# Kernel tuning notes

Measured on AMD Instinct MI355X. Metric: run time of the kernel, lower is better.

The kernel has to match this reference:

```python
import jax, jax.numpy as jnp
import numpy as np

TOP_K = 2

def setup_inputs() -> dict:
    key = jax.random.key(0)
    ks = jax.random.split(key, 5)
    B, S, H, F, E = 2, 1024, 2048, 4096, 8
    scale_h = 1.0 / np.sqrt(H)
    scale_f = 1.0 / np.sqrt(F)
    return {
        "hidden_states": jax.random.normal(ks[0], (B, S, H), dtype=jnp.float32),
        # nn.Linear weight layout is [out, in]
        "gate_w": jax.random.normal(ks[1], (E, H), dtype=jnp.float32) * scale_h,
        "w_gate": jax.random.normal(ks[2], (E, F, H), dtype=jnp.float32) * scale_h,
        "w_up": jax.random.normal(ks[3], (E, F, H), dtype=jnp.float32) * scale_h,
        "w_down": jax.random.normal(ks[4], (E, H, F), dtype=jnp.float32) * scale_f,
    }

def reference(hidden_states, gate_w, w_gate, w_up, w_down):
    B, S, H = hidden_states.shape
    E = gate_w.shape[0]
    x = hidden_states.reshape(-1, H)                     # [T, H]
    T = x.shape[0]
    # Router: softmax -> top-k -> renormalize
    router_logits = x @ gate_w.T                         # [T, E]
    routing_weights = jax.nn.softmax(router_logits, axis=-1)
    topk_w, topk_i = jax.lax.top_k(routing_weights, TOP_K)  # [T, k]
    topk_w = topk_w / jnp.sum(topk_w, axis=-1, keepdims=True)
    # Dense [T, E] combine weights (zero for non-selected experts);
    # equivalent math to the per-expert gather/scatter loop.
    dense_w = jnp.zeros((T, E), dtype=x.dtype).at[
        jnp.arange(T)[:, None], topk_i].set(topk_w)
    # SwiGLU experts, batched over E (grouped GEMM expressed densely)
    g = jnp.einsum('th,efh->tef', x, w_gate)             # [T, E, F]
    u = jnp.einsum('th,efh->tef', x, w_up)               # [T, E, F]
    h = jax.nn.silu(g) * u                               # [T, E, F]
    y = jnp.einsum('tef,ehf->teh', h, w_down)            # [T, E, H]
    out = jnp.einsum('te,teh->th', dense_w, y)           # [T, H]
    return out.reshape(B, S, H)
```

## Files before the change

kernel.cpp:

```cpp
#include <hip/hip_runtime.h>
#include <hip/hip_bf16.h>


#define T_TOK 2048
#define H_DIM 2048
#define F_DIM 4096
#define E_NUM 8
#define NPAIR (T_TOK * 2)

typedef __attribute__((ext_vector_type(8))) short short8;
typedef __attribute__((ext_vector_type(4))) float f32x4;

__device__ __forceinline__ unsigned short f2bf(float f) {
    unsigned u = __builtin_bit_cast(unsigned, f);
    u = (u + 0x7FFFu + ((u >> 16) & 1u)) >> 16;
    return (unsigned short)u;
}

__device__ __forceinline__ uint4 pack8(float4 a, float4 b) {
    uint4 o;
    o.x = f2bf(a.x) | ((unsigned)f2bf(a.y) << 16);
    o.y = f2bf(a.z) | ((unsigned)f2bf(a.w) << 16);
    o.z = f2bf(b.x) | ((unsigned)f2bf(b.y) << 16);
    o.w = f2bf(b.z) | ((unsigned)f2bf(b.w) << 16);
    return o;
}

__device__ __forceinline__ uint2 pack4(float4 a) {
    uint2 o;
    o.x = f2bf(a.x) | ((unsigned)f2bf(a.y) << 16);
    o.y = f2bf(a.z) | ((unsigned)f2bf(a.w) << 16);
    return o;
}

__device__ __forceinline__ void gload16(const void* g, void* s) {
    __builtin_amdgcn_global_load_lds(
        (const __attribute__((address_space(1))) unsigned int*)g,
        (__attribute__((address_space(3))) unsigned int*)s, 16, 0, 0);
}

__global__ void k_router(const float* __restrict__ x, const float* __restrict__ gw,
                         ushort* __restrict__ xb,
                         int2* __restrict__ eidx, float2* __restrict__ ew,
                         int* __restrict__ cnt) {
    int t = blockIdx.x * 4 + (threadIdx.x >> 6);
    int lane = threadIdx.x & 63;
    const float* xr = x + (size_t)t * H_DIM;
    ushort* xbr = xb + (size_t)t * H_DIM;

    #pragma unroll
    for (int j = 0; j < 4; j++) {
        int idx = (j * 64 + lane) * 8;
        const float4* p = (const float4*)(xr + idx);
        uint2 lo = pack4(p[0]), hi = pack4(p[1]);
        *(uint4*)(xbr + idx) = make_uint4(lo.x, lo.y, hi.x, hi.y);
    }

    float l[E_NUM];
    #pragma unroll
    for (int e = 0; e < E_NUM; e++) {
        const float* wr = gw + (size_t)e * H_DIM;
        float acc = 0.f;
        for (int i = lane; i < H_DIM; i += 64) acc += xr[i] * wr[i];
        #pragma unroll
        for (int o = 32; o; o >>= 1) acc += __shfl_xor(acc, o);
        l[e] = acc;
    }
    if (lane == 0) {
        int e0 = 0;
        #pragma unroll
        for (int e = 1; e < E_NUM; e++) if (l[e] > l[e0]) e0 = e;
        int e1 = -1;
        #pragma unroll
        for (int e = 0; e < E_NUM; e++) {
            if (e == e0) continue;
            if (e1 < 0 || l[e] > l[e1]) e1 = e;
        }
        float s1 = expf(l[e1] - l[e0]);
        float w0 = 1.f / (1.f + s1);
        float w1 = s1 * w0;
        eidx[t] = make_int2(e0, e1);
        ew[t]   = make_float2(w0, w1);
        atomicAdd(&cnt[e0], 1);
        atomicAdd(&cnt[e1], 1);
    }
}

__global__ void k_offfill(const int* __restrict__ cnt, int* __restrict__ off,
                          const int2* __restrict__ eidx,
                          int* __restrict__ ptok, int2* __restrict__ inv) {
    __shared__ int soff[E_NUM];
    __shared__ int scnt[E_NUM];
    if (threadIdx.x == 0) {
        int s = 0;
        for (int e = 0; e < E_NUM; e++) { soff[e] = s; off[e] = s; s += cnt[e]; scnt[e] = 0; }
        off[E_NUM] = s;
    }
    __syncthreads();
    for (int t = threadIdx.x; t < T_TOK; t += blockDim.x) {
        int2 e = eidx[t];
        int p0 = soff[e.x] + atomicAdd(&scnt[e.x], 1);
        ptok[p0] = t;
        int p1 = soff[e.y] + atomicAdd(&scnt[e.y], 1);
        ptok[p1] = t;
        inv[t] = make_int2(p0, p1);
    }
}

__global__ __launch_bounds__(512, 4) void k_gemm1(
        const ushort* __restrict__ xb, const float* __restrict__ wg,
        const float* __restrict__ wu, const int* __restrict__ ptok,
        const int* __restrict__ off, ushort* __restrict__ hbuf) {
    __shared__ __align__(16) ushort As[256 * 64];
    __shared__ __align__(16) ushort Bg[64 * 64];
    __shared__ __align__(16) ushort Bu[64 * 64];

    int e = blockIdx.y >> 3, mt = blockIdx.y & 7;
    int base = off[e], ne = off[e + 1] - base;
    int row0 = mt * 256;
    if (row0 >= ne) return;
    int nb = blockIdx.x * 64;

    int tid = threadIdx.x;
    int wv = tid >> 6, l = tid & 63;
    int lr = l & 15, lk = l >> 4;
    int wm = wv >> 1, wn = wv & 1;

    int wvu = __builtin_amdgcn_readfirstlane(wv);
    const ushort* srcA[4];
    int sslot = 8 * ((l & 7) ^ ((l >> 3) & 7));
    #pragma unroll
    for (int c = 0; c < 4; c++) {
        int r = (wvu * 4 + c) * 8 + (l >> 3);
        int pp = base + min(row0 + r, ne - 1);
        srcA[c] = xb + (size_t)ptok[pp] * H_DIM + sslot;
    }

    int brow = tid >> 3, bs = tid & 7;
    const float* wgrow = wg + ((size_t)e * F_DIM + nb + brow) * H_DIM + bs * 8;
    const float* wurow = wu + ((size_t)e * F_DIM + nb + brow) * H_DIM + bs * 8;
    int bo = brow * 64 + (((bs * 16) ^ ((brow & 7) << 4)) >> 1);

    int rsw = (lr & 7) << 4;

    f32x4 accg[4][2] = {}; f32x4 accu[4][2] = {};

    for (int kb = 0; kb < H_DIM; kb += 64) {
        __syncthreads();
        #pragma unroll
        for (int c = 0; c < 4; c++)
            gload16(srcA[c] + kb, (ushort*)As + (wvu * 4 + c) * 512);
        float4 g0 = *(const float4*)(wgrow + kb);
        float4 g1 = *(const float4*)(wgrow + kb + 4);
        *(uint4*)(&Bg[bo]) = pack8(g0, g1);
        float4 u0 = *(const float4*)(wurow + kb);
        float4 u1 = *(const float4*)(wurow + kb + 4);
        *(uint4*)(&Bu[bo]) = pack8(u0, u1);
        __syncthreads();

        #pragma unroll
        for (int kk = 0; kk < 2; kk++) {
            int kby = kk * 64 + lk * 16;
            short8 a[4];
            #pragma unroll
            for (int m = 0; m < 4; m++) {
                int row = wm * 64 + m * 16 + lr;
                a[m] = *(const short8*)(&As[(row * 128 + (kby ^ rsw)) >> 1]);
            }
            #pragma unroll
            for (int n = 0; n < 2; n++) {
                int rowb = wn * 32 + n * 16 + lr;
                int boff = (rowb * 128 + (kby ^ rsw)) >> 1;
                short8 bg8 = *(const short8*)(&Bg[boff]);
                short8 bu8 = *(const short8*)(&Bu[boff]);
                #pragma unroll
                for (int m = 0; m < 4; m++) {
                    accg[m][n] = __builtin_amdgcn_mfma_f32_16x16x32_bf16(a[m], bg8, accg[m][n], 0, 0, 0);
                    accu[m][n] = __builtin_amdgcn_mfma_f32_16x16x32_bf16(a[m], bu8, accu[m][n], 0, 0, 0);
                }
            }
        }
    }

    #pragma unroll
    for (int m = 0; m < 4; m++) {
        #pragma unroll
        for (int r = 0; r < 4; r++) {
            int lrow = wm * 64 + m * 16 + lk * 4 + r;
            if (row0 + lrow < ne) {
                size_t rb = (size_t)(base + row0 + lrow) * F_DIM + nb;
                #pragma unroll
                for (int n = 0; n < 2; n++) {
                    float g = accg[m][n][r], u = accu[m][n][r];
                    float hv = g / (1.f + __expf(-g)) * u;
                    hbuf[rb + wn * 32 + n * 16 + lr] = f2bf(hv);
                }
            }
        }
    }
}

__global__ __launch_bounds__(512, 2) void k_gemm2(
        const ushort* __restrict__ hbuf, const float* __restrict__ wd,
        const int* __restrict__ off, float* __restrict__ ybuf) {
    __shared__ __align__(16) ushort As[256 * 64];
    __shared__ __align__(16) ushort Bs[128 * 64];

    int e = blockIdx.y >> 3, mt = blockIdx.y & 7;
    int base = off[e], ne = off[e + 1] - base;
    int row0 = mt * 256;
    if (row0 >= ne) return;
    int nb = blockIdx.x * 128;

    int tid = threadIdx.x;
    int wv = tid >> 6, l = tid & 63;
    int lr = l & 15, lk = l >> 4;
    int wm = wv >> 1, wn = wv & 1;

    int wvu = __builtin_amdgcn_readfirstlane(wv);
    const ushort* srcA[4];
    int sslot = 8 * ((l & 7) ^ ((l >> 3) & 7));
    #pragma unroll
    for (int c = 0; c < 4; c++) {
        int r = (wvu * 4 + c) * 8 + (l >> 3);
        int pp = base + min(row0 + r, ne - 1);
        srcA[c] = hbuf + (size_t)pp * F_DIM + sslot;
    }

    int brow = tid >> 2, bs = tid & 3;
    const float* wdrow = wd + ((size_t)e * H_DIM + nb + brow) * F_DIM + bs * 16;
    int bsw = (brow & 7) << 4;
    int bo0 = brow * 64 + (((bs * 32) ^ bsw) >> 1);
    int bo1 = brow * 64 + (((bs * 32 + 16) ^ bsw) >> 1);

    int rsw = (lr & 7) << 4;

    f32x4 acc[4][4] = {};

    for (int kb = 0; kb < F_DIM; kb += 64) {
        __syncthreads();
        #pragma unroll
        for (int c = 0; c < 4; c++)
            gload16(srcA[c] + kb, (ushort*)As + (wvu * 4 + c) * 512);
        float4 b0 = *(const float4*)(wdrow + kb);
        float4 b1 = *(const float4*)(wdrow + kb + 4);
        float4 b2 = *(const float4*)(wdrow + kb + 8);
        float4 b3 = *(const float4*)(wdrow + kb + 12);
        *(uint4*)(&Bs[bo0]) = pack8(b0, b1);
        *(uint4*)(&Bs[bo1]) = pack8(b2, b3);
        __syncthreads();

        #pragma unroll
        for (int kk = 0; kk < 2; kk++) {
            int kby = kk * 64 + lk * 16;
            short8 a[4];
            #pragma unroll
            for (int m = 0; m < 4; m++) {
                int row = wm * 64 + m * 16 + lr;
                a[m] = *(const short8*)(&As[(row * 128 + (kby ^ rsw)) >> 1]);
            }
            #pragma unroll
            for (int n = 0; n < 4; n++) {
                int rowb = wn * 64 + n * 16 + lr;
                short8 b8 = *(const short8*)(&Bs[(rowb * 128 + (kby ^ rsw)) >> 1]);
                #pragma unroll
                for (int m = 0; m < 4; m++)
                    acc[m][n] = __builtin_amdgcn_mfma_f32_16x16x32_bf16(a[m], b8, acc[m][n], 0, 0, 0);
            }
        }
    }

    #pragma unroll
    for (int m = 0; m < 4; m++) {
        #pragma unroll
        for (int r = 0; r < 4; r++) {
            int lrow = wm * 64 + m * 16 + lk * 4 + r;
            if (row0 + lrow < ne) {
                float* yrow = ybuf + (size_t)(base + row0 + lrow) * H_DIM + nb;
                #pragma unroll
                for (int n = 0; n < 4; n++)
                    yrow[wn * 64 + n * 16 + lr] = acc[m][n][r];
            }
        }
    }
}

__global__ void k_combine(const float* __restrict__ ybuf,
                          const float2* __restrict__ ew,
                          const int2* __restrict__ inv,
                          float* __restrict__ out) {
    int t = blockIdx.x;
    float2 w = ew[t];
    int2 pp = inv[t];
    const float4* y0 = (const float4*)(ybuf + (size_t)pp.x * H_DIM);
    const float4* y1 = (const float4*)(ybuf + (size_t)pp.y * H_DIM);
    float4* o = (float4*)(out + (size_t)t * H_DIM);
    for (int j = threadIdx.x; j < H_DIM / 4; j += blockDim.x) {
        float4 a = y0[j], b = y1[j];
        float4 r;
        r.x = w.x * a.x + w.y * b.x;
        r.y = w.x * a.y + w.y * b.y;
        r.z = w.x * a.z + w.y * b.z;
        r.w = w.x * a.w + w.y * b.w;
        o[j] = r;
    }
}

extern "C" void kernel_launch(void* const* d_in, const int* in_sizes, int n_in,
                              void* d_out, int out_size, void* d_ws, size_t ws_size,
                              hipStream_t stream) {
    const float* x  = (const float*)d_in[0];
    const float* gw = (const float*)d_in[1];
    const float* wg = (const float*)d_in[2];
    const float* wu = (const float*)d_in[3];
    const float* wd = (const float*)d_in[4];
    float* out = (float*)d_out;

    char* ws = (char*)d_ws;
    size_t o = 0;
    ushort* xb   = (ushort*)(ws + o); o += (size_t)T_TOK * H_DIM * 2;
    ushort* hbuf = (ushort*)(ws + o); o += (size_t)NPAIR * F_DIM * 2;
    float*  ybuf = (float*) (ws + o); o += (size_t)NPAIR * H_DIM * 4;
    int*    ptok = (int*)   (ws + o); o += NPAIR * 4;
    int2*   eidx = (int2*)  (ws + o); o += T_TOK * 8;
    float2* ew   = (float2*)(ws + o); o += T_TOK * 8;
    int2*   inv  = (int2*)  (ws + o); o += T_TOK * 8;
    int*    cnt  = (int*)   (ws + o); o += 256;
    int*    off  = (int*)   (ws + o); o += 256;

    hipMemsetAsync(cnt, 0, 256, stream);

    k_router <<<T_TOK / 4, 256, 0, stream>>>(x, gw, xb, eidx, ew, cnt);
    k_offfill<<<1, 256, 0, stream>>>(cnt, off, eidx, ptok, inv);

    dim3 g1(F_DIM / 64, E_NUM * 8);
    k_gemm1<<<g1, 512, 0, stream>>>(xb, wg, wu, ptok, off, hbuf);
    dim3 g2(H_DIM / 128, E_NUM * 8);
    k_gemm2<<<g2, 512, 0, stream>>>(hbuf, wd, off, ybuf);
    k_combine<<<T_TOK, 256, 0, stream>>>(ybuf, ew, inv, out);
}
```

Before: 555.9 us.

## Split gate/up GEMM into two sequential phases with wider N tile

The fused gate/up GEMM is split into two sequential passes inside each block, each computing a 128-wide N tile with one B buffer. The gate result is stored as bf16 to hbuf and read back during the up pass to apply SiLU and multiply. Each A tile is reused across twice as many columns per pass, and accumulator register pressure stays about the same. The cost is that the gathered A rows are loaded twice (once per phase) and there is an extra global round-trip through hbuf. The gate value is also rounded to bf16 before SiLU.

```diff
diff --git a/kernel.cpp b/kernel.cpp
--- a/kernel.cpp
+++ b/kernel.cpp
@@ -15,6 +15,11 @@
     unsigned u = __builtin_bit_cast(unsigned, f);
     u = (u + 0x7FFFu + ((u >> 16) & 1u)) >> 16;
     return (unsigned short)u;
+}
+
+__device__ __forceinline__ float bf2f(unsigned short us) {
+    unsigned u = ((unsigned)us) << 16;
+    return __builtin_bit_cast(float, u);
 }
 
 __device__ __forceinline__ uint4 pack8(float4 a, float4 b) {
@@ -112,14 +117,13 @@
         const float* __restrict__ wu, const int* __restrict__ ptok,
         const int* __restrict__ off, ushort* __restrict__ hbuf) {
     __shared__ __align__(16) ushort As[256 * 64];
-    __shared__ __align__(16) ushort Bg[64 * 64];
-    __shared__ __align__(16) ushort Bu[64 * 64];
+    __shared__ __align__(16) ushort Bs[128 * 64];
 
     int e = blockIdx.y >> 3, mt = blockIdx.y & 7;
     int base = off[e], ne = off[e + 1] - base;
     int row0 = mt * 256;
     if (row0 >= ne) return;
-    int nb = blockIdx.x * 64;
+    int nb = blockIdx.x * 128;
 
     int tid = threadIdx.x;
     int wv = tid >> 6, l = tid & 63;
@@ -136,64 +140,70 @@
         srcA[c] = xb + (size_t)ptok[pp] * H_DIM + sslot;
     }
 
-    int brow = tid >> 3, bs = tid & 7;
-    const float* wgrow = wg + ((size_t)e * F_DIM + nb + brow) * H_DIM + bs * 8;
-    const float* wurow = wu + ((size_t)e * F_DIM + nb + brow) * H_DIM + bs * 8;
-    int bo = brow * 64 + (((bs * 16) ^ ((brow & 7) << 4)) >> 1);
+    int brow = tid >> 2, bs = tid & 3;
+    size_t woff = ((size_t)e * F_DIM + nb + brow) * H_DIM + bs * 16;
+    int bsw = (brow & 7) << 4;
+    int bo0 = brow * 64 + (((bs * 32) ^ bsw) >> 1);
+    int bo1 = brow * 64 + (((bs * 32 + 16) ^ bsw) >> 1);
 
     int rsw = (lr & 7) << 4;
 
-    f32x4 accg[4][2] = {}; f32x4 accu[4][2] = {};
-
-    for (int kb = 0; kb < H_DIM; kb += 64) {
-        __syncthreads();
-        #pragma unroll
-        for (int c = 0; c < 4; c++)
-            gload16(srcA[c] + kb, (ushort*)As + (wvu * 4 + c) * 512);
-        float4 g0 = *(const float4*)(wgrow + kb);
-        float4 g1 = *(const float4*)(wgrow + kb + 4);
-        *(uint4*)(&Bg[bo]) = pack8(g0, g1);
-        float4 u0 = *(const float4*)(wurow + kb);
-        float4 u1 = *(const float4*)(wurow + kb + 4);
-        *(uint4*)(&Bu[bo]) = pack8(u0, u1);
-        __syncthreads();
-
-        #pragma unroll
-        for (int kk = 0; kk < 2; kk++) {
-            int kby = kk * 64 + lk * 16;
-            short8 a[4];
-            #pragma unroll
-            for (int m = 0; m < 4; m++) {
-                int row = wm * 64 + m * 16 + lr;
-                a[m] = *(const short8*)(&As[(row * 128 + (kby ^ rsw)) >> 1]);
-            }
-            #pragma unroll
-            for (int n = 0; n < 2; n++) {
-                int rowb = wn * 32 + n * 16 + lr;
-                int boff = (rowb * 128 + (kby ^ rsw)) >> 1;
-                short8 bg8 = *(const short8*)(&Bg[boff]);
-                short8 bu8 = *(const short8*)(&Bu[boff]);
+    #pragma unroll 1
+    for (int ph = 0; ph < 2; ph++) {
+        const float* wrow = (ph ? wu : wg) + woff;
+        f32x4 acc[4][4] = {};
+
+        for (int kb = 0; kb < H_DIM; kb += 64) {
+            __syncthreads();
+            #pragma unroll
+            for (int c = 0; c < 4; c++)
+                gload16(srcA[c] + kb, (ushort*)As + (wvu * 4 + c) * 512);
+            float4 b0 = *(const float4*)(wrow + kb);
+            float4 b1 = *(const float4*)(wrow + kb + 4);
+            float4 b2 = *(const float4*)(wrow + kb + 8);
+            float4 b3 = *(const float4*)(wrow + kb + 12);
+            *(uint4*)(&Bs[bo0]) = pack8(b0, b1);
+            *(uint4*)(&Bs[bo1]) = pack8(b2, b3);
+            __syncthreads();
+
+            #pragma unroll
+            for (int kk = 0; kk < 2; kk++) {
+                int kby = kk * 64 + lk * 16;
+                short8 a[4];
                 #pragma unroll
                 for (int m = 0; m < 4; m++) {
-                    accg[m][n] = __builtin_amdgcn_mfma_f32_16x16x32_bf16(a[m], bg8, accg[m][n], 0, 0, 0);
-                    accu[m][n] = __builtin_amdgcn_mfma_f32_16x16x32_bf16(a[m], bu8, accu[m][n], 0, 0, 0);
+                    int row = wm * 64 + m * 16 + lr;
+                    a[m] = *(const short8*)(&As[(row * 128 + (kby ^ rsw)) >> 1]);
                 }
-            }
-        }
-    }
-
-    #pragma unroll
-    for (int m = 0; m < 4; m++) {
-        #pragma unroll
-        for (int r = 0; r < 4; r++) {
-            int lrow = wm * 64 + m * 16 + lk * 4 + r;
-            if (row0 + lrow < ne) {
-                size_t rb = (size_t)(base + row0 + lrow) * F_DIM + nb;
                 #pragma unroll
-                for (int n = 0; n < 2; n++) {
-                    float g = accg[m][n][r], u = accu[m][n][r];
-                    float hv = g / (1.f + __expf(-g)) * u;
-                    hbuf[rb + wn * 32 + n * 16 + lr] = f2bf(hv);
+                for (int n = 0; n < 4; n++) {
+                    int rowb = wn * 64 + n * 16 + lr;
+                    short8 b8 = *(const short8*)(&Bs[(rowb * 128 + (kby ^ rsw)) >> 1]);
+                    #pragma unroll
+                    for (int m = 0; m < 4; m++)
+                        acc[m][n] = __builtin_amdgcn_mfma_f32_16x16x32_bf16(a[m], b8, acc[m][n], 0, 0, 0);
+                }
+            }
+        }
+
+        #pragma unroll
+        for (int m = 0; m < 4; m++) {
+            #pragma unroll
+            for (int r = 0; r < 4; r++) {
+                int lrow = wm * 64 + m * 16 + lk * 4 + r;
+                if (row0 + lrow < ne) {
+                    ushort* hb = hbuf + (size_t)(base + row0 + lrow) * F_DIM + nb;
+                    #pragma unroll
+                    for (int n = 0; n < 4; n++) {
+                        int col = wn * 64 + n * 16 + lr;
+                        if (ph == 0) {
+                            hb[col] = f2bf(acc[m][n][r]);
+                        } else {
+                            float g = bf2f(hb[col]);
+                            float u = acc[m][n][r];
+                            hb[col] = f2bf(g / (1.f + __expf(-g)) * u);
+                        }
+                    }
                 }
             }
         }
@@ -333,7 +343,7 @@
     k_router <<<T_TOK / 4, 256, 0, stream>>>(x, gw, xb, eidx, ew, cnt);
     k_offfill<<<1, 256, 0, stream>>>(cnt, off, eidx, ptok, inv);
 
-    dim3 g1(F_DIM / 64, E_NUM * 8);
+    dim3 g1(F_DIM / 128, E_NUM * 8);
     k_gemm1<<<g1, 512, 0, stream>>>(xb, wg, wu, ptok, off, hbuf);
     dim3 g2(H_DIM / 128, E_NUM * 8);
     k_gemm2<<<g2, 512, 0, stream>>>(hbuf, wd, off, ybuf);
```

New measurement: 699.7 us. 1.26x slower.
